# Kernel tuning notes

Measured on AMD Instinct MI355X. Metric: run time of the kernel, lower is better.

Reference implementation:

```python
import jax, jax.numpy as jnp
import numpy as np

T, H, F, E, K = 2048, 1024, 1024, 8, 2  # tokens, hidden, ffn, experts, top_k


def setup_inputs() -> dict:
    key = jax.random.key(0)
    k1, k2, k3, k4, k5 = jax.random.split(key, 5)
    hidden_states = jax.random.normal(k1, (T, H), dtype=jnp.float32)
    # router outputs: positive weights (renormalize=False in module, used as-is)
    topk_weights = jax.random.uniform(k2, (T, K), dtype=jnp.float32)
    topk_ids = jax.random.randint(k3, (T, K), 0, E, dtype=jnp.int32)
    # gate_up: (E, 2F, H) with first F rows = gate, last F rows = up
    gate_up_weight = jax.random.normal(k4, (E, 2 * F, H), dtype=jnp.float32) * 0.02
    # down: (E, H, F)
    down_weight = jax.random.normal(k5, (E, H, F), dtype=jnp.float32) * 0.02
    return {
        'hidden_states': hidden_states,
        'topk_weights': topk_weights,
        'topk_ids': topk_ids,
        'gate_up_weight': gate_up_weight,
        'down_weight': down_weight,
    }


def reference(hidden_states, topk_weights, topk_ids, gate_up_weight, down_weight):
    # Fused MoE: per selected expert, y = (silu(x@Wg^T) * (x@Wu^T)) @ Wd^T,
    # combined with router weights (renormalize=False).
    f = down_weight.shape[-1]
    # [T, E, 2F]: gate_up projection for every expert (dense ref for grouped GEMM)
    gu = jnp.einsum('th,eoh->teo', hidden_states, gate_up_weight)
    gate, up = gu[..., :f], gu[..., f:]
    act = jax.nn.silu(gate) * up                     # [T, E, F]
    y = jnp.einsum('tef,ehf->teh', act, down_weight)  # [T, E, H]
    # gather the top-k experts per token and combine
    y_sel = jnp.take_along_axis(y, topk_ids[:, :, None], axis=1)  # [T, K, H]
    out = jnp.sum(y_sel * topk_weights[:, :, None], axis=1)       # [T, H]
    return out.astype(hidden_states.dtype)
```

## Files before the change

### kernel.cpp

```cpp
#include <hip/hip_runtime.h>
#include <hip/hip_bf16.h>

#define T_TOK 2048
#define HID   1024
#define FF    1024
#define NEXP  8
#define NPAIR 4096

#define BM 128
#define BK 32
#define MAX_MT 40
#define MAXROWS (MAX_MT*BM)
#define PPT (NPAIR/256)

using bf16x8 = __attribute__((ext_vector_type(8))) __bf16;
using f32x4  = __attribute__((ext_vector_type(4))) float;
using us8    = __attribute__((ext_vector_type(8))) unsigned short;

__device__ __forceinline__ unsigned short f2bf(float f) {
    unsigned int u = __float_as_uint(f);
    return (unsigned short)((u + 0x7FFF + ((u >> 16) & 1)) >> 16);
}
__device__ __forceinline__ float bf2f(unsigned short s) {
    return __uint_as_float(((unsigned int)s) << 16);
}
__device__ __forceinline__ void gll16(const unsigned short* g, unsigned short* l) {
    __builtin_amdgcn_global_load_lds(
        (const __attribute__((address_space(1))) void*)(const void*)g,
        (__attribute__((address_space(3))) void*)(void*)l, 16, 0, 0);
}

__global__ void prep_kernel(const float* __restrict__ hs,
                            const int* __restrict__ ids,
                            int* __restrict__ pair_pos,
                            int* __restrict__ row_tok,
                            int* __restrict__ meta,
                            unsigned short* __restrict__ hs_b) {
    int tid = threadIdx.x;
    if (blockIdx.x == 1024) {
        __shared__ int S[2][256][NEXP];
        __shared__ int base[NEXP];
        int myc[NEXP];
        int eloc[PPT];
#pragma unroll
        for (int e = 0; e < NEXP; e++) myc[e] = 0;
#pragma unroll
        for (int i = 0; i < PPT; i++) {
            int e = ids[tid * PPT + i];
            eloc[i] = e;
#pragma unroll
            for (int ee = 0; ee < NEXP; ee++) myc[ee] += (e == ee);
        }
#pragma unroll
        for (int e = 0; e < NEXP; e++) S[0][tid][e] = myc[e];
        __syncthreads();
        int src = 0;
        for (int d = 1; d < 256; d <<= 1) {
#pragma unroll
            for (int e = 0; e < NEXP; e++) {
                int v = S[src][tid][e];
                if (tid >= d) v += S[src][tid - d][e];
                S[src ^ 1][tid][e] = v;
            }
            __syncthreads();
            src ^= 1;
        }
        if (tid == 0) {
            int mt = 0;
            for (int e = 0; e < NEXP; e++) {
                meta[e] = mt;
                base[e] = mt * BM;
                mt += (S[src][255][e] + BM - 1) / BM;
            }
            meta[NEXP] = mt;
        }
        for (int i = tid; i < MAXROWS; i += 256) row_tok[i] = -1;
        __syncthreads();
        int off[NEXP];
#pragma unroll
        for (int e = 0; e < NEXP; e++) off[e] = base[e] + S[src][tid][e] - myc[e];
#pragma unroll
        for (int i = 0; i < PPT; i++) {
            int p = tid * PPT + i;
            int e = eloc[i];
            int pos = 0;
#pragma unroll
            for (int ee = 0; ee < NEXP; ee++) if (e == ee) pos = off[ee]++;
            pair_pos[p] = pos;
            row_tok[pos] = p >> 1;
        }
        return;
    }
    long stride = 1024L * 256;
    long t0 = (long)blockIdx.x * 256 + tid;
    const long NH = (long)T_TOK * HID / 4;
    for (long i = t0; i < NH; i += stride) {
        float4 v = ((const float4*)hs)[i];
        ushort4 o; o.x = f2bf(v.x); o.y = f2bf(v.y); o.z = f2bf(v.z); o.w = f2bf(v.w);
        ((ushort4*)hs_b)[i] = o;
    }
}

template<int EPI, int NBY, int BN>
__global__ __launch_bounds__(256)
void gemm_moe(const unsigned short* __restrict__ A,
              const float* __restrict__ B,
              unsigned short* __restrict__ Cbf,
              const int* __restrict__ meta,
              const int* __restrict__ row_tok,
              int K, long Bexp) {
    constexpr int NJ = BN / 32;
    constexpr int NBCH = (BN * BK) / (8 * 256);
    __shared__ unsigned short As[2][BM * BK];
    __shared__ unsigned short Bs[2][BN * BK];

    int L = blockIdx.x;
    int xcd = L & 7;
    int slot = L >> 3;
    constexpr int PER = NBY / 8;
    int by = xcd * PER + (slot % PER);
    int bx = slot / PER;
    if (bx >= meta[NEXP]) return;
    int e = 0;
#pragma unroll
    for (int i = 1; i < NEXP; i++) if (bx >= meta[i]) e = i;

    long m0 = (long)bx * BM;
    int n0 = by * BN;
    const float* Bb = B + (long)e * Bexp;

    int tid = threadIdx.x, lane = tid & 63, wv = tid >> 6;
    const int r = lane & 15;
    const int q = lane >> 4;
    const int mw = (wv >> 1) * 64, nw = (wv & 1) * (BN / 2);
    const int sw = (q ^ ((r >> 1) & 3)) * 8;

    const unsigned short* ap[2];
#pragma unroll
    for (int h = 0; h < 2; h++) {
        int c = h * 256 + tid;
        int row = c >> 2, cp = c & 3;
        int cc = cp ^ ((row >> 1) & 3);
        long grow;
        if (EPI == 1) {
            int tk = row_tok[m0 + row];
            if (tk < 0) tk = 0;
            grow = tk;
        } else {
            grow = m0 + row;
        }
        ap[h] = A + grow * (long)K + cc * 8;
    }
    const float* bp[NBCH];
#pragma unroll
    for (int h = 0; h < NBCH; h++) {
        int c = h * 256 + tid;
        int row = c >> 2, cp = c & 3;
        int cc = cp ^ ((row >> 1) & 3);
        long grow;
        if (EPI == 1) grow = ((row & 1) ? FF : 0) + ((n0 + row) >> 1);
        else          grow = n0 + row;
        bp[h] = Bb + grow * (long)K + cc * 8;
    }

    float4 br[NBCH][2];
    auto bload = [&](int k0) {
#pragma unroll
        for (int h = 0; h < NBCH; h++) {
            br[h][0] = *(const float4*)(bp[h] + k0);
            br[h][1] = *(const float4*)(bp[h] + k0 + 4);
        }
    };
    auto bwrite = [&](int s) {
#pragma unroll
        for (int h = 0; h < NBCH; h++) {
            us8 o;
            o[0] = f2bf(br[h][0].x); o[1] = f2bf(br[h][0].y);
            o[2] = f2bf(br[h][0].z); o[3] = f2bf(br[h][0].w);
            o[4] = f2bf(br[h][1].x); o[5] = f2bf(br[h][1].y);
            o[6] = f2bf(br[h][1].z); o[7] = f2bf(br[h][1].w);
            *(us8*)&Bs[s][(h * 256 + tid) * 8] = o;
        }
    };
    auto stageA = [&](int s, int k0) {
#pragma unroll
        for (int h = 0; h < 2; h++)
            gll16(ap[h] + k0, &As[s][(h * 256 + tid) * 8]);
    };

    f32x4 acc[4][NJ] = {};
    const int NKI = K / BK;
    bload(0);
    stageA(0, 0);
    bwrite(0);
    for (int ki = 0; ki < NKI; ki++) {
        __syncthreads();
        int s = ki & 1;
        if (ki + 1 < NKI) {
            bload((ki + 1) * BK);
            stageA(s ^ 1, (ki + 1) * BK);
        }
        bf16x8 a[4], b[NJ];
#pragma unroll
        for (int i = 0; i < 4; i++)
            a[i] = *(const bf16x8*)&As[s][(mw + i * 16 + r) * BK + sw];
#pragma unroll
        for (int j = 0; j < NJ; j++)
            b[j] = *(const bf16x8*)&Bs[s][(nw + j * 16 + r) * BK + sw];
#pragma unroll
        for (int i = 0; i < 4; i++)
#pragma unroll
            for (int j = 0; j < NJ; j++)
                acc[i][j] = __builtin_amdgcn_mfma_f32_16x16x32_bf16(a[i], b[j], acc[i][j], 0, 0, 0);
        if (ki + 1 < NKI) bwrite(s ^ 1);
        __syncthreads();
    }

    if (EPI == 1) {
#pragma unroll
        for (int i = 0; i < 4; i++) {
            long rowb = m0 + mw + i * 16 + q * 4;
#pragma unroll
            for (int j = 0; j < NJ; j++) {
                int n = n0 + nw + j * 16 + r;
#pragma unroll
                for (int reg = 0; reg < 4; reg++) {
                    float v = acc[i][j][reg];
                    float o = __shfl_xor(v, 1);
                    if (!(r & 1)) {
                        float g = v, u = o;
                        float s2 = g / (1.f + __expf(-g)) * u;
                        Cbf[(rowb + reg) * (long)FF + (n >> 1)] = f2bf(s2);
                    }
                }
            }
        }
    } else {
#pragma unroll
        for (int i = 0; i < 4; i++) {
            long rowb = m0 + mw + i * 16 + q * 4;
#pragma unroll
            for (int j = 0; j < NJ; j++) {
                int n = n0 + nw + j * 16 + r;
#pragma unroll
                for (int reg = 0; reg < 4; reg++)
                    Cbf[(rowb + reg) * (long)HID + n] = f2bf(acc[i][j][reg]);
            }
        }
    }
}

__global__ void combine_kernel(const unsigned short* __restrict__ y,
                               const float* __restrict__ tw,
                               const int* __restrict__ pair_pos,
                               float* __restrict__ out) {
    int t = blockIdx.x;
    int c = threadIdx.x * 4;
    int p0 = pair_pos[t * 2], p1 = pair_pos[t * 2 + 1];
    float w0 = tw[t * 2], w1 = tw[t * 2 + 1];
    ushort4 a = *(const ushort4*)(y + (long)p0 * HID + c);
    ushort4 b = *(const ushort4*)(y + (long)p1 * HID + c);
    float4 o;
    o.x = w0 * bf2f(a.x) + w1 * bf2f(b.x);
    o.y = w0 * bf2f(a.y) + w1 * bf2f(b.y);
    o.z = w0 * bf2f(a.z) + w1 * bf2f(b.z);
    o.w = w0 * bf2f(a.w) + w1 * bf2f(b.w);
    *(float4*)(out + (long)t * HID + c) = o;
}

extern "C" void kernel_launch(void* const* d_in, const int* in_sizes, int n_in,
                              void* d_out, int out_size, void* d_ws, size_t ws_size,
                              hipStream_t stream) {
    const float* hs  = (const float*)d_in[0];
    const float* tw  = (const float*)d_in[1];
    const int*   ids = (const int*)d_in[2];
    const float* wgu = (const float*)d_in[3];
    const float* wdn = (const float*)d_in[4];
    float* out = (float*)d_out;

    char* ws = (char*)d_ws;
    size_t off = 0;
    auto alloc = [&](size_t bytes) -> void* {
        void* p = ws + off;
        off += (bytes + 255) & ~(size_t)255;
        return p;
    };
    unsigned short* hs_b  = (unsigned short*)alloc((size_t)T_TOK * HID * 2);
    unsigned short* act   = (unsigned short*)alloc((size_t)MAXROWS * FF * 2);
    unsigned short* ybuf  = (unsigned short*)alloc((size_t)MAXROWS * HID * 2);
    int* pair_pos = (int*)alloc(NPAIR * 4);
    int* row_tok  = (int*)alloc(MAXROWS * 4);
    int* meta     = (int*)alloc(64);

    prep_kernel<<<1025, 256, 0, stream>>>(hs, ids, pair_pos, row_tok, meta, hs_b);

    gemm_moe<1, 16, 128><<<16 * MAX_MT, 256, 0, stream>>>(
        hs_b, wgu, act, meta, row_tok, HID, (long)(2 * FF) * HID);

    gemm_moe<2, 8, 128><<<8 * MAX_MT, 256, 0, stream>>>(
        act, wdn, ybuf, meta, row_tok, FF, (long)HID * FF);

    combine_kernel<<<T_TOK, 256, 0, stream>>>(ybuf, tw, pair_pos, out);
}
```

Measured before the change: 220.9 us.

## Triple-buffer MoE GEMM with two-stage-ahead prefetch and explicit waitcnt

The grouped GEMM moves from a double-buffered LDS pipeline to a triple-buffered one. B (fp32 weight) loads are issued two k-steps ahead into alternating register sets, and A is staged with direct global-to-LDS loads. Hand-placed s_waitcnt vmcnt immediates replace one of the two barriers per k-step. The prep kernel's hidden-state conversion now uses 256 blocks, each converting a contiguous chunk with 16-byte stores. The cost is more LDS and registers per block, and correctness depends on the hardcoded vmcnt counts matching the number of loads issued per stage.

```diff
diff --git a/kernel.cpp b/kernel.cpp
--- a/kernel.cpp
+++ b/kernel.cpp
@@ -28,6 +28,15 @@
     __builtin_amdgcn_global_load_lds(
         (const __attribute__((address_space(1))) void*)(const void*)g,
         (__attribute__((address_space(3))) void*)(void*)l, 16, 0, 0);
+}
+__device__ __forceinline__ ushort4 cvt4(float4 v) {
+    ushort4 o; o.x = f2bf(v.x); o.y = f2bf(v.y); o.z = f2bf(v.z); o.w = f2bf(v.w);
+    return o;
+}
+template<int N> __device__ __forceinline__ void wait_vm_lgkm0() {
+    if constexpr (N == 0)      asm volatile("s_waitcnt vmcnt(0) lgkmcnt(0)" ::: "memory");
+    else if constexpr (N == 2) asm volatile("s_waitcnt vmcnt(2) lgkmcnt(0)" ::: "memory");
+    else                       asm volatile("s_waitcnt vmcnt(6) lgkmcnt(0)" ::: "memory");
 }
 
 __global__ void prep_kernel(const float* __restrict__ hs,
@@ -37,67 +46,76 @@
                             int* __restrict__ meta,
                             unsigned short* __restrict__ hs_b) {
     int tid = threadIdx.x;
-    if (blockIdx.x == 1024) {
-        __shared__ int S[2][256][NEXP];
-        __shared__ int base[NEXP];
-        int myc[NEXP];
-        int eloc[PPT];
-#pragma unroll
-        for (int e = 0; e < NEXP; e++) myc[e] = 0;
-#pragma unroll
-        for (int i = 0; i < PPT; i++) {
-            int e = ids[tid * PPT + i];
-            eloc[i] = e;
-#pragma unroll
-            for (int ee = 0; ee < NEXP; ee++) myc[ee] += (e == ee);
-        }
-#pragma unroll
-        for (int e = 0; e < NEXP; e++) S[0][tid][e] = myc[e];
+    int bid = blockIdx.x;
+    if (bid < 256) {
+        long f4 = (long)bid * 2048 + tid * 2;
+        float4 v[8];
+#pragma unroll
+        for (int k = 0; k < 4; k++) {
+            v[2 * k]     = ((const float4*)hs)[f4 + k * 512];
+            v[2 * k + 1] = ((const float4*)hs)[f4 + k * 512 + 1];
+        }
+        long u8i = (long)bid * 1024 + tid;
+#pragma unroll
+        for (int k = 0; k < 4; k++) {
+            ushort4 lo = cvt4(v[2 * k]), hi = cvt4(v[2 * k + 1]);
+            us8 o;
+            o[0] = lo.x; o[1] = lo.y; o[2] = lo.z; o[3] = lo.w;
+            o[4] = hi.x; o[5] = hi.y; o[6] = hi.z; o[7] = hi.w;
+            ((us8*)hs_b)[u8i + k * 256] = o;
+        }
+        return;
+    }
+    __shared__ int S[2][256][NEXP];
+    __shared__ int base[NEXP];
+    int myc[NEXP];
+    int eloc[PPT];
+#pragma unroll
+    for (int e = 0; e < NEXP; e++) myc[e] = 0;
+#pragma unroll
+    for (int i = 0; i < PPT; i++) {
+        int e = ids[tid * PPT + i];
+        eloc[i] = e;
+#pragma unroll
+        for (int ee = 0; ee < NEXP; ee++) myc[ee] += (e == ee);
+    }
+#pragma unroll
+    for (int e = 0; e < NEXP; e++) S[0][tid][e] = myc[e];
+    __syncthreads();
+    int src = 0;
+    for (int d = 1; d < 256; d <<= 1) {
+#pragma unroll
+        for (int e = 0; e < NEXP; e++) {
+            int v = S[src][tid][e];
+            if (tid >= d) v += S[src][tid - d][e];
+            S[src ^ 1][tid][e] = v;
+        }
         __syncthreads();
-        int src = 0;
-        for (int d = 1; d < 256; d <<= 1) {
-#pragma unroll
-            for (int e = 0; e < NEXP; e++) {
-                int v = S[src][tid][e];
-                if (tid >= d) v += S[src][tid - d][e];
-                S[src ^ 1][tid][e] = v;
-            }
-            __syncthreads();
-            src ^= 1;
-        }
-        if (tid == 0) {
-            int mt = 0;
-            for (int e = 0; e < NEXP; e++) {
-                meta[e] = mt;
-                base[e] = mt * BM;
-                mt += (S[src][255][e] + BM - 1) / BM;
-            }
-            meta[NEXP] = mt;
-        }
-        for (int i = tid; i < MAXROWS; i += 256) row_tok[i] = -1;
-        __syncthreads();
-        int off[NEXP];
-#pragma unroll
-        for (int e = 0; e < NEXP; e++) off[e] = base[e] + S[src][tid][e] - myc[e];
-#pragma unroll
-        for (int i = 0; i < PPT; i++) {
-            int p = tid * PPT + i;
-            int e = eloc[i];
-            int pos = 0;
-#pragma unroll
-            for (int ee = 0; ee < NEXP; ee++) if (e == ee) pos = off[ee]++;
-            pair_pos[p] = pos;
-            row_tok[pos] = p >> 1;
-        }
-        return;
-    }
-    long stride = 1024L * 256;
-    long t0 = (long)blockIdx.x * 256 + tid;
-    const long NH = (long)T_TOK * HID / 4;
-    for (long i = t0; i < NH; i += stride) {
-        float4 v = ((const float4*)hs)[i];
-        ushort4 o; o.x = f2bf(v.x); o.y = f2bf(v.y); o.z = f2bf(v.z); o.w = f2bf(v.w);
-        ((ushort4*)hs_b)[i] = o;
+        src ^= 1;
+    }
+    if (tid == 0) {
+        int mt = 0;
+        for (int e = 0; e < NEXP; e++) {
+            meta[e] = mt;
+            base[e] = mt * BM;
+            mt += (S[src][255][e] + BM - 1) / BM;
+        }
+        meta[NEXP] = mt;
+    }
+    for (int i = tid; i < MAXROWS; i += 256) row_tok[i] = -1;
+    __syncthreads();
+    int off[NEXP];
+#pragma unroll
+    for (int e = 0; e < NEXP; e++) off[e] = base[e] + S[src][tid][e] - myc[e];
+#pragma unroll
+    for (int i = 0; i < PPT; i++) {
+        int p = tid * PPT + i;
+        int e = eloc[i];
+        int pos = 0;
+#pragma unroll
+        for (int ee = 0; ee < NEXP; ee++) if (e == ee) pos = off[ee]++;
+        pair_pos[p] = pos;
+        row_tok[pos] = p >> 1;
     }
 }
 
@@ -110,10 +128,13 @@
               const int* __restrict__ row_tok,
               int K, long Bexp) {
     constexpr int NJ = BN / 32;
+    constexpr int ACH = (BM * BK) / (8 * 256);
     constexpr int NBCH = (BN * BK) / (8 * 256);
-    __shared__ unsigned short As[2][BM * BK];
-    __shared__ unsigned short Bs[2][BN * BK];
-
+    static_assert(ACH == 2 && NBCH == 2, "vmcnt immediates assume 6 loads/stage");
+    __shared__ unsigned short As[3][BM * BK];
+    __shared__ unsigned short Bs[3][BN * BK];
+
+    int tid = threadIdx.x;
     int L = blockIdx.x;
     int xcd = L & 7;
     int slot = L >> 3;
@@ -129,15 +150,15 @@
     int n0 = by * BN;
     const float* Bb = B + (long)e * Bexp;
 
-    int tid = threadIdx.x, lane = tid & 63, wv = tid >> 6;
+    int lane = tid & 63, wv = tid >> 6;
     const int r = lane & 15;
     const int q = lane >> 4;
     const int mw = (wv >> 1) * 64, nw = (wv & 1) * (BN / 2);
     const int sw = (q ^ ((r >> 1) & 3)) * 8;
 
-    const unsigned short* ap[2];
-#pragma unroll
-    for (int h = 0; h < 2; h++) {
+    const unsigned short* ap[ACH];
+#pragma unroll
+    for (int h = 0; h < ACH; h++) {
         int c = h * 256 + tid;
         int row = c >> 2, cp = c & 3;
         int cc = cp ^ ((row >> 1) & 3);
@@ -163,58 +184,64 @@
         bp[h] = Bb + grow * (long)K + cc * 8;
     }
 
-    float4 br[NBCH][2];
-    auto bload = [&](int k0) {
-#pragma unroll
-        for (int h = 0; h < NBCH; h++) {
-            br[h][0] = *(const float4*)(bp[h] + k0);
-            br[h][1] = *(const float4*)(bp[h] + k0 + 4);
-        }
-    };
-    auto bwrite = [&](int s) {
-#pragma unroll
-        for (int h = 0; h < NBCH; h++) {
-            us8 o;
-            o[0] = f2bf(br[h][0].x); o[1] = f2bf(br[h][0].y);
-            o[2] = f2bf(br[h][0].z); o[3] = f2bf(br[h][0].w);
-            o[4] = f2bf(br[h][1].x); o[5] = f2bf(br[h][1].y);
-            o[6] = f2bf(br[h][1].z); o[7] = f2bf(br[h][1].w);
-            *(us8*)&Bs[s][(h * 256 + tid) * 8] = o;
-        }
-    };
-    auto stageA = [&](int s, int k0) {
-#pragma unroll
-        for (int h = 0; h < 2; h++)
-            gll16(ap[h] + k0, &As[s][(h * 256 + tid) * 8]);
-    };
-
     f32x4 acc[4][NJ] = {};
     const int NKI = K / BK;
-    bload(0);
-    stageA(0, 0);
-    bwrite(0);
-    for (int ki = 0; ki < NKI; ki++) {
-        __syncthreads();
-        int s = ki & 1;
-        if (ki + 1 < NKI) {
-            bload((ki + 1) * BK);
-            stageA(s ^ 1, (ki + 1) * BK);
-        }
-        bf16x8 a[4], b[NJ];
-#pragma unroll
-        for (int i = 0; i < 4; i++)
-            a[i] = *(const bf16x8*)&As[s][(mw + i * 16 + r) * BK + sw];
-#pragma unroll
-        for (int j = 0; j < NJ; j++)
-            b[j] = *(const bf16x8*)&Bs[s][(nw + j * 16 + r) * BK + sw];
-#pragma unroll
-        for (int i = 0; i < 4; i++)
-#pragma unroll
-            for (int j = 0; j < NJ; j++)
-                acc[i][j] = __builtin_amdgcn_mfma_f32_16x16x32_bf16(a[i], b[j], acc[i][j], 0, 0, 0);
-        if (ki + 1 < NKI) bwrite(s ^ 1);
-        __syncthreads();
-    }
+    float4 brA[2 * NBCH], brB[2 * NBCH];
+
+#define BLOADS(SET, K0) \
+    _Pragma("unroll") for (int h = 0; h < NBCH; h++) { \
+        SET[2*h]   = *(const float4*)(bp[h] + (K0)); \
+        SET[2*h+1] = *(const float4*)(bp[h] + (K0) + 4); }
+#define BWRITE(SET, SBUF) \
+    _Pragma("unroll") for (int h = 0; h < NBCH; h++) { \
+        us8 o_; \
+        o_[0]=f2bf(SET[2*h].x);   o_[1]=f2bf(SET[2*h].y); \
+        o_[2]=f2bf(SET[2*h].z);   o_[3]=f2bf(SET[2*h].w); \
+        o_[4]=f2bf(SET[2*h+1].x); o_[5]=f2bf(SET[2*h+1].y); \
+        o_[6]=f2bf(SET[2*h+1].z); o_[7]=f2bf(SET[2*h+1].w); \
+        *(us8*)&Bs[SBUF][(h * 256 + tid) * 8] = o_; }
+#define AGLL(SBUF, K0) \
+    _Pragma("unroll") for (int h = 0; h < ACH; h++) \
+        gll16(ap[h] + (K0), &As[SBUF][(h * 256 + tid) * 8]);
+#define BODY(KI, LD, CV, VM) do { \
+    wait_vm_lgkm0<VM>(); \
+    __builtin_amdgcn_s_barrier(); \
+    __builtin_amdgcn_sched_barrier(0); \
+    int sb_ = (KI) % 3; \
+    if ((KI) + 2 < NKI) { \
+        int sn_ = ((KI) + 2) % 3; \
+        BLOADS(LD, ((KI) + 2) * BK); \
+        AGLL(sn_, ((KI) + 2) * BK); \
+    } \
+    bf16x8 a_[4], b_[NJ]; \
+    _Pragma("unroll") for (int i = 0; i < 4; i++) \
+        a_[i] = *(const bf16x8*)&As[sb_][(mw + i * 16 + r) * BK + sw]; \
+    _Pragma("unroll") for (int j = 0; j < NJ; j++) \
+        b_[j] = *(const bf16x8*)&Bs[sb_][(nw + j * 16 + r) * BK + sw]; \
+    if ((KI) + 1 < NKI) { int sw_ = ((KI) + 1) % 3; BWRITE(CV, sw_); } \
+    _Pragma("unroll") for (int i = 0; i < 4; i++) \
+    _Pragma("unroll") for (int j = 0; j < NJ; j++) \
+        acc[i][j] = __builtin_amdgcn_mfma_f32_16x16x32_bf16(a_[i], b_[j], acc[i][j], 0, 0, 0); \
+} while (0)
+
+    BLOADS(brA, 0);
+    BLOADS(brB, BK);
+    AGLL(0, 0);
+    AGLL(1, BK);
+    BWRITE(brA, 0);
+
+    BODY(0, brA, brB, 0);
+    BODY(1, brB, brA, 6);
+    for (int ki = 2; ki < NKI - 2; ki += 2) {
+        BODY(ki,     brA, brB, 6);
+        BODY(ki + 1, brB, brA, 6);
+    }
+    BODY(NKI - 2, brA, brB, 6);
+    BODY(NKI - 1, brB, brA, 0);
+#undef BODY
+#undef AGLL
+#undef BWRITE
+#undef BLOADS
 
     if (EPI == 1) {
 #pragma unroll
@@ -292,7 +319,7 @@
     int* row_tok  = (int*)alloc(MAXROWS * 4);
     int* meta     = (int*)alloc(64);
 
-    prep_kernel<<<1025, 256, 0, stream>>>(hs, ids, pair_pos, row_tok, meta, hs_b);
+    prep_kernel<<<257, 256, 0, stream>>>(hs, ids, pair_pos, row_tok, meta, hs_b);
 
     gemm_moe<1, 16, 128><<<16 * MAX_MT, 256, 0, stream>>>(
         hs_b, wgu, act, meta, row_tok, HID, (long)(2 * FF) * HID);
```

After: 240.4 us. +8.9%, slower.

## Stage fp32 weights into LDS via direct global-to-LDS loads, convert at fragment read

Applied to the files above, without the earlier changes.

The GEMM kernels now copy fp32 weight tiles straight into shared memory with global_load_lds, using an XOR swizzle. Previously each tile went through registers, was converted to bf16 in registers, then written to LDS. The bf16 conversion now happens when MFMA fragments are read from LDS, so weight prefetch no longer ties up VGPRs or needs explicit store instructions. The cost is a B tile in LDS twice as large, plus conversion work repeated by every wave that reads the same B rows. The prep kernel is also reorganised into 256 conversion blocks of 8 float4s per thread, plus one routing block.

```diff
diff --git a/kernel.cpp b/kernel.cpp
--- a/kernel.cpp
+++ b/kernel.cpp
@@ -28,6 +28,15 @@
     __builtin_amdgcn_global_load_lds(
         (const __attribute__((address_space(1))) void*)(const void*)g,
         (__attribute__((address_space(3))) void*)(void*)l, 16, 0, 0);
+}
+__device__ __forceinline__ void gll16f(const float* g, float* l) {
+    __builtin_amdgcn_global_load_lds(
+        (const __attribute__((address_space(1))) void*)(const void*)g,
+        (__attribute__((address_space(3))) void*)(void*)l, 16, 0, 0);
+}
+__device__ __forceinline__ ushort4 cvt4(float4 v) {
+    ushort4 o; o.x = f2bf(v.x); o.y = f2bf(v.y); o.z = f2bf(v.z); o.w = f2bf(v.w);
+    return o;
 }
 
 __global__ void prep_kernel(const float* __restrict__ hs,
@@ -37,67 +46,76 @@
                             int* __restrict__ meta,
                             unsigned short* __restrict__ hs_b) {
     int tid = threadIdx.x;
-    if (blockIdx.x == 1024) {
-        __shared__ int S[2][256][NEXP];
-        __shared__ int base[NEXP];
-        int myc[NEXP];
-        int eloc[PPT];
-#pragma unroll
-        for (int e = 0; e < NEXP; e++) myc[e] = 0;
-#pragma unroll
-        for (int i = 0; i < PPT; i++) {
-            int e = ids[tid * PPT + i];
-            eloc[i] = e;
-#pragma unroll
-            for (int ee = 0; ee < NEXP; ee++) myc[ee] += (e == ee);
-        }
-#pragma unroll
-        for (int e = 0; e < NEXP; e++) S[0][tid][e] = myc[e];
+    int bid = blockIdx.x;
+    if (bid < 256) {
+        long f4 = (long)bid * 2048 + tid * 2;
+        float4 v[8];
+#pragma unroll
+        for (int k = 0; k < 4; k++) {
+            v[2 * k]     = ((const float4*)hs)[f4 + k * 512];
+            v[2 * k + 1] = ((const float4*)hs)[f4 + k * 512 + 1];
+        }
+        long u8i = (long)bid * 1024 + tid;
+#pragma unroll
+        for (int k = 0; k < 4; k++) {
+            ushort4 lo = cvt4(v[2 * k]), hi = cvt4(v[2 * k + 1]);
+            us8 o;
+            o[0] = lo.x; o[1] = lo.y; o[2] = lo.z; o[3] = lo.w;
+            o[4] = hi.x; o[5] = hi.y; o[6] = hi.z; o[7] = hi.w;
+            ((us8*)hs_b)[u8i + k * 256] = o;
+        }
+        return;
+    }
+    __shared__ int S[2][256][NEXP];
+    __shared__ int base[NEXP];
+    int myc[NEXP];
+    int eloc[PPT];
+#pragma unroll
+    for (int e = 0; e < NEXP; e++) myc[e] = 0;
+#pragma unroll
+    for (int i = 0; i < PPT; i++) {
+        int e = ids[tid * PPT + i];
+        eloc[i] = e;
+#pragma unroll
+        for (int ee = 0; ee < NEXP; ee++) myc[ee] += (e == ee);
+    }
+#pragma unroll
+    for (int e = 0; e < NEXP; e++) S[0][tid][e] = myc[e];
+    __syncthreads();
+    int src = 0;
+    for (int d = 1; d < 256; d <<= 1) {
+#pragma unroll
+        for (int e = 0; e < NEXP; e++) {
+            int v = S[src][tid][e];
+            if (tid >= d) v += S[src][tid - d][e];
+            S[src ^ 1][tid][e] = v;
+        }
         __syncthreads();
-        int src = 0;
-        for (int d = 1; d < 256; d <<= 1) {
-#pragma unroll
-            for (int e = 0; e < NEXP; e++) {
-                int v = S[src][tid][e];
-                if (tid >= d) v += S[src][tid - d][e];
-                S[src ^ 1][tid][e] = v;
-            }
-            __syncthreads();
-            src ^= 1;
-        }
-        if (tid == 0) {
-            int mt = 0;
-            for (int e = 0; e < NEXP; e++) {
-                meta[e] = mt;
-                base[e] = mt * BM;
-                mt += (S[src][255][e] + BM - 1) / BM;
-            }
-            meta[NEXP] = mt;
-        }
-        for (int i = tid; i < MAXROWS; i += 256) row_tok[i] = -1;
-        __syncthreads();
-        int off[NEXP];
-#pragma unroll
-        for (int e = 0; e < NEXP; e++) off[e] = base[e] + S[src][tid][e] - myc[e];
-#pragma unroll
-        for (int i = 0; i < PPT; i++) {
-            int p = tid * PPT + i;
-            int e = eloc[i];
-            int pos = 0;
-#pragma unroll
-            for (int ee = 0; ee < NEXP; ee++) if (e == ee) pos = off[ee]++;
-            pair_pos[p] = pos;
-            row_tok[pos] = p >> 1;
-        }
-        return;
-    }
-    long stride = 1024L * 256;
-    long t0 = (long)blockIdx.x * 256 + tid;
-    const long NH = (long)T_TOK * HID / 4;
-    for (long i = t0; i < NH; i += stride) {
-        float4 v = ((const float4*)hs)[i];
-        ushort4 o; o.x = f2bf(v.x); o.y = f2bf(v.y); o.z = f2bf(v.z); o.w = f2bf(v.w);
-        ((ushort4*)hs_b)[i] = o;
+        src ^= 1;
+    }
+    if (tid == 0) {
+        int mt = 0;
+        for (int e = 0; e < NEXP; e++) {
+            meta[e] = mt;
+            base[e] = mt * BM;
+            mt += (S[src][255][e] + BM - 1) / BM;
+        }
+        meta[NEXP] = mt;
+    }
+    for (int i = tid; i < MAXROWS; i += 256) row_tok[i] = -1;
+    __syncthreads();
+    int off[NEXP];
+#pragma unroll
+    for (int e = 0; e < NEXP; e++) off[e] = base[e] + S[src][tid][e] - myc[e];
+#pragma unroll
+    for (int i = 0; i < PPT; i++) {
+        int p = tid * PPT + i;
+        int e = eloc[i];
+        int pos = 0;
+#pragma unroll
+        for (int ee = 0; ee < NEXP; ee++) if (e == ee) pos = off[ee]++;
+        pair_pos[p] = pos;
+        row_tok[pos] = p >> 1;
     }
 }
 
@@ -110,10 +128,12 @@
               const int* __restrict__ row_tok,
               int K, long Bexp) {
     constexpr int NJ = BN / 32;
-    constexpr int NBCH = (BN * BK) / (8 * 256);
+    constexpr int ACH = (BM * BK) / (8 * 256);
+    constexpr int BCH = (BN * 8) / 256;
     __shared__ unsigned short As[2][BM * BK];
-    __shared__ unsigned short Bs[2][BN * BK];
-
+    __shared__ float          BsF[2][BN * BK];
+
+    int tid = threadIdx.x;
     int L = blockIdx.x;
     int xcd = L & 7;
     int slot = L >> 3;
@@ -129,15 +149,15 @@
     int n0 = by * BN;
     const float* Bb = B + (long)e * Bexp;
 
-    int tid = threadIdx.x, lane = tid & 63, wv = tid >> 6;
+    int lane = tid & 63, wv = tid >> 6;
     const int r = lane & 15;
     const int q = lane >> 4;
     const int mw = (wv >> 1) * 64, nw = (wv & 1) * (BN / 2);
     const int sw = (q ^ ((r >> 1) & 3)) * 8;
 
-    const unsigned short* ap[2];
-#pragma unroll
-    for (int h = 0; h < 2; h++) {
+    const unsigned short* ap[ACH];
+#pragma unroll
+    for (int h = 0; h < ACH; h++) {
         int c = h * 256 + tid;
         int row = c >> 2, cp = c & 3;
         int cc = cp ^ ((row >> 1) & 3);
@@ -151,68 +171,57 @@
         }
         ap[h] = A + grow * (long)K + cc * 8;
     }
-    const float* bp[NBCH];
-#pragma unroll
-    for (int h = 0; h < NBCH; h++) {
+    const float* bp[BCH];
+#pragma unroll
+    for (int h = 0; h < BCH; h++) {
         int c = h * 256 + tid;
-        int row = c >> 2, cp = c & 3;
-        int cc = cp ^ ((row >> 1) & 3);
+        int row = c >> 3, pos = c & 7;
+        int srcc = pos ^ (row & 7);
         long grow;
         if (EPI == 1) grow = ((row & 1) ? FF : 0) + ((n0 + row) >> 1);
         else          grow = n0 + row;
-        bp[h] = Bb + grow * (long)K + cc * 8;
-    }
-
-    float4 br[NBCH][2];
-    auto bload = [&](int k0) {
-#pragma unroll
-        for (int h = 0; h < NBCH; h++) {
-            br[h][0] = *(const float4*)(bp[h] + k0);
-            br[h][1] = *(const float4*)(bp[h] + k0 + 4);
-        }
-    };
-    auto bwrite = [&](int s) {
-#pragma unroll
-        for (int h = 0; h < NBCH; h++) {
-            us8 o;
-            o[0] = f2bf(br[h][0].x); o[1] = f2bf(br[h][0].y);
-            o[2] = f2bf(br[h][0].z); o[3] = f2bf(br[h][0].w);
-            o[4] = f2bf(br[h][1].x); o[5] = f2bf(br[h][1].y);
-            o[6] = f2bf(br[h][1].z); o[7] = f2bf(br[h][1].w);
-            *(us8*)&Bs[s][(h * 256 + tid) * 8] = o;
-        }
-    };
-    auto stageA = [&](int s, int k0) {
-#pragma unroll
-        for (int h = 0; h < 2; h++)
+        bp[h] = Bb + grow * (long)K + srcc * 4;
+    }
+
+    auto stage = [&](int s, int k0) {
+#pragma unroll
+        for (int h = 0; h < ACH; h++)
             gll16(ap[h] + k0, &As[s][(h * 256 + tid) * 8]);
+#pragma unroll
+        for (int h = 0; h < BCH; h++)
+            gll16f(bp[h] + k0, &BsF[s][(h * 256 + tid) * 4]);
     };
 
     f32x4 acc[4][NJ] = {};
     const int NKI = K / BK;
-    bload(0);
-    stageA(0, 0);
-    bwrite(0);
+    stage(0, 0);
     for (int ki = 0; ki < NKI; ki++) {
         __syncthreads();
+        if (ki + 1 < NKI) stage((ki + 1) & 1, (ki + 1) * BK);
         int s = ki & 1;
-        if (ki + 1 < NKI) {
-            bload((ki + 1) * BK);
-            stageA(s ^ 1, (ki + 1) * BK);
-        }
         bf16x8 a[4], b[NJ];
 #pragma unroll
         for (int i = 0; i < 4; i++)
             a[i] = *(const bf16x8*)&As[s][(mw + i * 16 + r) * BK + sw];
 #pragma unroll
-        for (int j = 0; j < NJ; j++)
-            b[j] = *(const bf16x8*)&Bs[s][(nw + j * 16 + r) * BK + sw];
+        for (int j = 0; j < NJ; j++) {
+            int R = nw + j * 16 + r;
+            int m = R & 7;
+            const float* bs_ = &BsF[s][R * 32];
+            f32x4 lo = *(const f32x4*)&bs_[((2 * q) ^ m) << 2];
+            f32x4 hi = *(const f32x4*)&bs_[((2 * q + 1) ^ m) << 2];
+            bf16x8 bb;
+            bb[0] = (__bf16)lo[0]; bb[1] = (__bf16)lo[1];
+            bb[2] = (__bf16)lo[2]; bb[3] = (__bf16)lo[3];
+            bb[4] = (__bf16)hi[0]; bb[5] = (__bf16)hi[1];
+            bb[6] = (__bf16)hi[2]; bb[7] = (__bf16)hi[3];
+            b[j] = bb;
+        }
 #pragma unroll
         for (int i = 0; i < 4; i++)
 #pragma unroll
             for (int j = 0; j < NJ; j++)
                 acc[i][j] = __builtin_amdgcn_mfma_f32_16x16x32_bf16(a[i], b[j], acc[i][j], 0, 0, 0);
-        if (ki + 1 < NKI) bwrite(s ^ 1);
         __syncthreads();
     }
 
@@ -292,7 +301,7 @@
     int* row_tok  = (int*)alloc(MAXROWS * 4);
     int* meta     = (int*)alloc(64);
 
-    prep_kernel<<<1025, 256, 0, stream>>>(hs, ids, pair_pos, row_tok, meta, hs_b);
+    prep_kernel<<<257, 256, 0, stream>>>(hs, ids, pair_pos, row_tok, meta, hs_b);
 
     gemm_moe<1, 16, 128><<<16 * MAX_MT, 256, 0, stream>>>(
         hs_b, wgu, act, meta, row_tok, HID, (long)(2 * FF) * HID);
```

After: 218.3 us. Within noise of the previous version (-1.1%).
